# Optimization experiments

Hardware: AMD Instinct MI355X
Metric: run time of the kernel (lower is better)

Reference implementation:

```python
import jax, jax.numpy as jnp
import numpy as np

PAD = 2  # kernel_height // 2 for kernel_height=5


def earth_pad2d(x, ph, pw):
    # circular pad in longitude (last dim), zero pad in latitude (dim 2)
    if pw > 0:
        x = jnp.concatenate([x[..., -pw:], x, x[..., :pw]], axis=-1)
    if ph > 0:
        x = jnp.pad(x, ((0, 0), (0, 0), (ph, ph), (0, 0)))
    return x


def earth_wrap2d(x, w, pad):
    # fold circular overhang of a transposed-conv output back onto width w
    core = x[..., pad:pad + w]
    rw = x.shape[-1] - pad - w  # right overhang (stride-1... here 1)
    core = core.at[..., :rw].add(x[..., pad + w:])
    core = core.at[..., w - pad:].add(x[..., :pad])
    return core


def _conv(x, w, b, stride):
    # torch Conv2d, weight [Cout, Cin, 1, k], VALID padding, stride (1, stride)
    y = jax.lax.conv_general_dilated(x, w, (1, stride), 'VALID',
                                     dimension_numbers=('NCHW', 'OIHW', 'NCHW'))
    return y + b[None, :, None, None]


def _convT(x, w, stride):
    # torch ConvTranspose2d (no bias), weight [Cin, Cout, 1, k], padding 0
    k = w.shape[-1]
    wr = jnp.transpose(jnp.flip(w, axis=(2, 3)), (1, 0, 2, 3))  # -> [Cout, Cin, 1, k]
    return jax.lax.conv_general_dilated(x, wr, (1, 1),
                                        [(0, 0), (k - 1, k - 1)],
                                        lhs_dilation=(1, stride),
                                        dimension_numbers=('NCHW', 'OIHW', 'NCHW'))


def _edge(x, d, p):
    return x[:, :, -p:, :] if d == 1 else x[:, :, :p, :]


def _set_edge(x, d, p, v):
    return x.at[:, :, -p:, :].set(v) if d == 1 else x.at[:, :, :p, :].set(v)


def _forward(strips, wi, wo):
    strips_pad = [earth_pad2d(s, PAD, PAD) for s in strips]
    # center strip inner edges from the adjacent coarser strips (to_inners[0])
    for d in (-1, 1):
        a = _edge(strips[2 + d], -d, PAD)
        a = _convT(a, wi[0], 2)
        a = earth_wrap2d(a, strips[2].shape[3], 2)
        a = earth_pad2d(a, 0, PAD)
        strips_pad[2] = _set_edge(strips_pad[2], d, PAD, a)
    # outer strips: far edge from next coarser (to_inners), near edge from finer (to_outers)
    for mi in (1, 2):
        for d in (-1, 1):
            idx = 2 + d * mi
            sp = strips_pad[idx]
            if mi + 1 <= 2:
                o = _edge(strips[2 + d * (mi + 1)], -d, PAD)
                o = _convT(o, wi[mi], 2)
                o = earth_wrap2d(o, strips[idx].shape[3], 2)
                o = earth_pad2d(o, 0, PAD)
                sp = _set_edge(sp, d, PAD, o)
            en = _edge(strips[2 + d * (mi - 1)], d, PAD)
            en = earth_pad2d(en, 0, 2)
            en = _conv(en, wo[mi - 1][0], wo[mi - 1][1], 2)
            en = earth_pad2d(en, 0, PAD)
            sp = _set_edge(sp, -d, PAD, en)
            strips_pad[idx] = sp
    return tuple(strips_pad)


def setup_inputs():
    key = jax.random.key(0)
    ks = jax.random.split(key, 11)
    B, C, W = 1, 256, 1440
    shapes = [(B, C, 30, W // 4), (B, C, 60, W // 2), (B, C, 180, W),
              (B, C, 60, W // 2), (B, C, 30, W // 4)]
    d = {}
    for i, sh in enumerate(shapes):
        d['s%d' % i] = jax.random.normal(ks[i], sh, dtype=jnp.float32)
    scale = 0.03
    d['wi0'] = jax.random.normal(ks[5], (C, C, 1, 5), dtype=jnp.float32) * scale
    d['wi1'] = jax.random.normal(ks[6], (C, C, 1, 5), dtype=jnp.float32) * scale
    d['wo0'] = jax.random.normal(ks[7], (C, C, 1, 5), dtype=jnp.float32) * scale
    d['bo0'] = jax.random.normal(ks[8], (C,), dtype=jnp.float32) * 0.01
    d['wo1'] = jax.random.normal(ks[9], (C, C, 1, 5), dtype=jnp.float32) * scale
    d['bo1'] = jax.random.normal(ks[10], (C,), dtype=jnp.float32) * 0.01
    return d


def reference(s0, s1, s2, s3, s4, wi0, wi1, wo0, bo0, wo1, bo1):
    return _forward([s0, s1, s2, s3, s4], [wi0, wi1], [(wo0, bo0), (wo1, bo1)])
```

## Files before the change

### kernel.cpp

```cpp
#include <hip/hip_runtime.h>


struct ConvJob {
  const float* x; const float* wt; const float* bias; float* out;
  int Hin, Win, r0, Hout, Wcore, h0, blk_start;
};
struct ConvParams { ConvJob j[8]; };

struct CopyParams {
  const float* in0; const float* in1; const float* in2; const float* in3; const float* in4;
  float* o0; float* o1; float* o2; float* o3; float* o4;
};

struct WTParams { const float* src[4]; float* dst[4]; };

__global__ __launch_bounds__(256) void transpose_all_kernel(WTParams p) {
  int b = blockIdx.x;
  int which = b / 1280;
  int idx = (b - which * 1280) * 256 + threadIdx.x;
  int hi = idx >> 10;
  int icq = hi / 5;
  int k = hi - icq * 5;
  int lo = idx & 1023;
  int oc = lo >> 2;
  int icr = lo & 3;
  int ic = icq * 4 + icr;
  const float* s = p.src[which];
  float v = (which < 2) ? s[(ic * 256 + oc) * 5 + k] : s[(oc * 256 + ic) * 5 + k];
  p.dst[which][idx] = v;
}


template <int NOUT, int NCC>
__device__ __forceinline__ void conv_unit(const ConvJob jb, int local, int t, float* xs,
                                          float bv) {
  int tile = local >> 1;
  int r = local & 1;
  const int Win = jb.Win;
  const int Hout = jb.Hout;
  const float* xrow = jb.x + ((size_t)(t * jb.Hin + jb.r0 + r)) * Win;
  const float* wq = jb.wt + t * 4;
  const int Wop = jb.Wcore + 4;
  float* orow = jb.out + ((size_t)(t * Hout + jb.h0 + r)) * Wop;

  int base0;
  if (NOUT == 8) base0 = 2 * (tile * 8) - 2;
  else           base0 = tile * 8 - 1;
#pragma unroll
  for (int cc = 0; cc < NCC; ++cc) {
    int col = base0 + cc;
    col += (col < 0) ? Win : 0;
    col -= (col >= Win) ? Win : 0;
    xs[cc * 256 + t] = xrow[col];
  }
  __syncthreads();

  float acc[NOUT];
#pragma unroll
  for (int i = 0; i < NOUT; ++i) acc[i] = bv;

#pragma unroll 1
  for (int icq = 0; icq < 64; ++icq) {
    float4 wv[5];
#pragma unroll
    for (int k = 0; k < 5; ++k)
      wv[k] = *(const float4*)(wq + (size_t)(icq * 5 + k) * 1024);
    int ic0 = icq * 4;
#pragma unroll
    for (int cc = 0; cc < NCC; ++cc) {
      float4 xq = *(const float4*)&xs[cc * 256 + ic0];
#pragma unroll
      for (int i = 0; i < NOUT; ++i) {
        int k = (NOUT == 8) ? (cc - 2 * i) : (i + 4 - 2 * cc);
        if (k >= 0 && k < 5) {
          float4 w = wv[k];
          acc[i] += w.x * xq.x + w.y * xq.y + w.z * xq.z + w.w * xq.w;
        }
      }
    }
  }

  __syncthreads();
#pragma unroll
  for (int i = 0; i < NOUT; ++i) xs[i * 257 + t] = acc[i];
  __syncthreads();
  constexpr int SL = NOUT / 2;
  constexpr int OCR = 256 / SL;
  constexpr int RND = 256 / OCR;
  int g0 = (NOUT == 8) ? tile * 8 : tile * 16;
#pragma unroll
  for (int q = 0; q < RND; ++q) {
    int oc = (t / SL) + q * OCR;
    int s = t & (SL - 1);
    float2 v = make_float2(xs[(2 * s) * 257 + oc], xs[(2 * s + 1) * 257 + oc]);
    *(float2*)(jb.out + ((size_t)(oc * Hout + jb.h0 + r)) * Wop + 2 + g0 + 2 * s) = v;
  }
  if (tile == 0) {
    orow[jb.Wcore + 2] = xs[0 * 257 + t];
    orow[jb.Wcore + 3] = xs[1 * 257 + t];
  }
  if (g0 + NOUT == jb.Wcore) {
    orow[0] = xs[(NOUT - 2) * 257 + t];
    orow[1] = xs[(NOUT - 1) * 257 + t];
  }
}

__global__ __launch_bounds__(256, 4) void conv_kernel(ConvParams p) {
  __shared__ float xs[19 * 256];
  int bx = blockIdx.x;
  int t = threadIdx.x;
  if (bx < 540) {
    int ji = (bx >= 450) ? 3 : (bx >= 360) ? 2 : (bx >= 180) ? 1 : 0;
    conv_unit<16, 10>(p.j[ji], bx - p.j[ji].blk_start, t, xs, 0.f);
  } else {
    int j2 = (bx >= 990) ? 7 : (bx >= 900) ? 6 : (bx >= 720) ? 5 : 4;
    conv_unit<8, 19>(p.j[j2], bx - p.j[j2].blk_start, t, xs, p.j[j2].bias[t]);
  }
}


__device__ __forceinline__ float4 pack4(float2 a, float2 b) {
  return make_float4(a.x, a.y, b.x, b.y);
}

template <int H, int W>
__device__ __forceinline__ void copy_row(const float* __restrict__ in,
                                         float* __restrict__ out, int rl, int lane) {
  constexpr int CORE = W / 4;
  int c = rl / H;
  const float* src = in + (size_t)rl * W;
  float* dst = out + (size_t)(rl + c * 4 + 2) * (W + 4);
  int w4 = 1 + lane;
  while (w4 < CORE) {
    int w4b = w4 + 64;
    float2 a0 = *(const float2*)(src + w4 * 4 - 2);
    float2 b0 = *(const float2*)(src + w4 * 4);
    if (w4b < CORE) {
      float2 a1 = *(const float2*)(src + w4b * 4 - 2);
      float2 b1 = *(const float2*)(src + w4b * 4);
      *(float4*)(dst + w4 * 4) = pack4(a0, b0);
      *(float4*)(dst + w4b * 4) = pack4(a1, b1);
    } else {
      *(float4*)(dst + w4 * 4) = pack4(a0, b0);
    }
    w4 += 128;
  }
  if (lane == 0) {
    float2 E = *(const float2*)(src + W - 2);
    float2 F = *(const float2*)(src);
    float4 v = pack4(E, F);
    *(float4*)(dst) = v;
    *(float4*)(dst + W) = v;
  }
}

__device__ __forceinline__ void zero_row(const CopyParams& p, int z, int lane) {
  int strip = z >> 9, cr = z & 511, c = cr >> 1, r = cr & 1;
  float* dst = strip ? p.o4 + (size_t)(c * 34 + 32 + r) * 364
                     : p.o0 + (size_t)(c * 34 + r) * 364;
  for (int w4 = lane; w4 < 91; w4 += 64)
    *(float4*)(dst + w4 * 4) = make_float4(0.f, 0.f, 0.f, 0.f);
}

__device__ __forceinline__ void do_row(const CopyParams& p, int gid, int lane) {
  if (gid < 46080)      copy_row<180, 1440>(p.in2, p.o2, gid, lane);
  else if (gid < 61440) copy_row<60, 720>(p.in1, p.o1, gid - 46080, lane);
  else if (gid < 76800) copy_row<60, 720>(p.in3, p.o3, gid - 61440, lane);
  else if (gid < 84480) copy_row<30, 360>(p.in0, p.o0, gid - 76800, lane);
  else if (gid < 92160) copy_row<30, 360>(p.in4, p.o4, gid - 84480, lane);
  else                  zero_row(p, gid - 92160, lane);
}

__global__ __launch_bounds__(256, 8) void copy_kernel(CopyParams p) {
  int wid = blockIdx.x * 4 + (threadIdx.x >> 6);
  int lane = threadIdx.x & 63;
  for (int gid = wid; gid < 93184; gid += 8192) do_row(p, gid, lane);
}

extern "C" void kernel_launch(void* const* d_in, const int* in_sizes, int n_in,
                              void* d_out, int out_size, void* d_ws, size_t ws_size,
                              hipStream_t stream) {
  const float* s0 = (const float*)d_in[0];
  const float* s1 = (const float*)d_in[1];
  const float* s2 = (const float*)d_in[2];
  const float* s3 = (const float*)d_in[3];
  const float* s4 = (const float*)d_in[4];
  const float* wi0 = (const float*)d_in[5];
  const float* wi1 = (const float*)d_in[6];
  const float* wo0 = (const float*)d_in[7];
  const float* bo0 = (const float*)d_in[8];
  const float* wo1 = (const float*)d_in[9];
  const float* bo1 = (const float*)d_in[10];

  float* out = (float*)d_out;
  float* out0 = out;
  float* out1 = out + 3168256;
  float* out2 = out + 15030272;
  float* out3 = out + 83048448;
  float* out4 = out + 94910464;

  float* wt0 = (float*)d_ws;
  float* wt1 = wt0 + 327680;
  float* wt2 = wt1 + 327680;
  float* wt3 = wt2 + 327680;

  WTParams wp;
  wp.src[0] = wi0; wp.src[1] = wi1; wp.src[2] = wo0; wp.src[3] = wo1;
  wp.dst[0] = wt0; wp.dst[1] = wt1; wp.dst[2] = wt2; wp.dst[3] = wt3;
  transpose_all_kernel<<<5120, 256, 0, stream>>>(wp);

  ConvParams cp;
  cp.j[0] = {s1, wt0, nullptr, out2,  60,  720,  58, 184, 1440,   0,   0};
  cp.j[1] = {s3, wt0, nullptr, out2,  60,  720,   0, 184, 1440, 182, 180};
  cp.j[2] = {s0, wt1, nullptr, out1,  30,  360,  28,  64,  720,   0, 360};
  cp.j[3] = {s4, wt1, nullptr, out3,  30,  360,   0,  64,  720,  62, 450};
  cp.j[4] = {s2, wt2, bo0,     out1, 180, 1440,   0,  64,  720,  62, 540};
  cp.j[5] = {s2, wt2, bo0,     out3, 180, 1440, 178,  64,  720,   0, 720};
  cp.j[6] = {s1, wt3, bo1,     out0,  60,  720,   0,  34,  360,  32, 900};
  cp.j[7] = {s3, wt3, bo1,     out4,  60,  720,  58,  34,  360,   0, 990};
  conv_kernel<<<1080, 256, 0, stream>>>(cp);

  CopyParams kp;
  kp.in0 = s0; kp.in1 = s1; kp.in2 = s2; kp.in3 = s3; kp.in4 = s4;
  kp.o0 = out0; kp.o1 = out1; kp.o2 = out2; kp.o3 = out3; kp.o4 = out4;
  copy_kernel<<<2048, 256, 0, stream>>>(kp);
}
```

Before: 322.6 us.

## Process both edge rows per block, interleave jobs, and prefetch weights

Each conv block now computes both output rows of an edge strip, so every weight float4 loaded is reused for two rows instead of one. Blocks are interleaved across the eight jobs, and tile widths are chosen per job so all jobs use the same number of tiles (720 blocks instead of 1080). The next channel-quad's weights are register-prefetched while the current quad is computed. This doubles the accumulators and the shared-memory footprint, and launch bounds drop occupancy to 2 blocks per SM.

```diff
diff --git a/kernel.cpp b/kernel.cpp
--- a/kernel.cpp
+++ b/kernel.cpp
@@ -3,7 +3,7 @@
 
 struct ConvJob {
   const float* x; const float* wt; const float* bias; float* out;
-  int Hin, Win, r0, Hout, Wcore, h0, blk_start;
+  int Hin, Win, r0, Hout, Wcore, h0;
 };
 struct ConvParams { ConvJob j[8]; };
 
@@ -31,71 +31,26 @@
 }
 
 
-template <int NOUT, int NCC>
-__device__ __forceinline__ void conv_unit(const ConvJob jb, int local, int t, float* xs,
-                                          float bv) {
-  int tile = local >> 1;
-  int r = local & 1;
-  const int Win = jb.Win;
-  const int Hout = jb.Hout;
-  const float* xrow = jb.x + ((size_t)(t * jb.Hin + jb.r0 + r)) * Win;
-  const float* wq = jb.wt + t * 4;
-  const int Wop = jb.Wcore + 4;
-  float* orow = jb.out + ((size_t)(t * Hout + jb.h0 + r)) * Wop;
-
-  int base0;
-  if (NOUT == 8) base0 = 2 * (tile * 8) - 2;
-  else           base0 = tile * 8 - 1;
-#pragma unroll
-  for (int cc = 0; cc < NCC; ++cc) {
-    int col = base0 + cc;
-    col += (col < 0) ? Win : 0;
-    col -= (col >= Win) ? Win : 0;
-    xs[cc * 256 + t] = xrow[col];
-  }
-  __syncthreads();
-
-  float acc[NOUT];
-#pragma unroll
-  for (int i = 0; i < NOUT; ++i) acc[i] = bv;
-
-#pragma unroll 1
-  for (int icq = 0; icq < 64; ++icq) {
-    float4 wv[5];
-#pragma unroll
-    for (int k = 0; k < 5; ++k)
-      wv[k] = *(const float4*)(wq + (size_t)(icq * 5 + k) * 1024);
-    int ic0 = icq * 4;
-#pragma unroll
-    for (int cc = 0; cc < NCC; ++cc) {
-      float4 xq = *(const float4*)&xs[cc * 256 + ic0];
-#pragma unroll
-      for (int i = 0; i < NOUT; ++i) {
-        int k = (NOUT == 8) ? (cc - 2 * i) : (i + 4 - 2 * cc);
-        if (k >= 0 && k < 5) {
-          float4 w = wv[k];
-          acc[i] += w.x * xq.x + w.y * xq.y + w.z * xq.z + w.w * xq.w;
-        }
-      }
-    }
-  }
-
+template <int NOUT>
+__device__ __forceinline__ void epilogue_row(const ConvJob& jb, int g0, int t, int r,
+                                             const float* acc, float* xs) {
   __syncthreads();
 #pragma unroll
   for (int i = 0; i < NOUT; ++i) xs[i * 257 + t] = acc[i];
   __syncthreads();
   constexpr int SL = NOUT / 2;
   constexpr int OCR = 256 / SL;
-  constexpr int RND = 256 / OCR;
-  int g0 = (NOUT == 8) ? tile * 8 : tile * 16;
-#pragma unroll
-  for (int q = 0; q < RND; ++q) {
+  const int Hout = jb.Hout;
+  const int Wop = jb.Wcore + 4;
+#pragma unroll
+  for (int q = 0; q < SL; ++q) {
     int oc = (t / SL) + q * OCR;
     int s = t & (SL - 1);
     float2 v = make_float2(xs[(2 * s) * 257 + oc], xs[(2 * s + 1) * 257 + oc]);
     *(float2*)(jb.out + ((size_t)(oc * Hout + jb.h0 + r)) * Wop + 2 + g0 + 2 * s) = v;
   }
-  if (tile == 0) {
+  float* orow = jb.out + ((size_t)(t * Hout + jb.h0 + r)) * Wop;
+  if (g0 == 0) {
     orow[jb.Wcore + 2] = xs[0 * 257 + t];
     orow[jb.Wcore + 3] = xs[1 * 257 + t];
   }
@@ -105,16 +60,80 @@
   }
 }
 
-__global__ __launch_bounds__(256, 4) void conv_kernel(ConvParams p) {
-  __shared__ float xs[19 * 256];
+template <int NOUT, int NCC, bool TR>
+__device__ __forceinline__ void conv2(const ConvJob jb, int tile, int t, float* xs,
+                                      float bv) {
+  const int Win = jb.Win;
+  int g0 = tile * NOUT;
+  int base0 = TR ? (g0 >> 1) - 1 : 2 * g0 - 2;
+
+#pragma unroll
+  for (int r = 0; r < 2; ++r) {
+    const float* xrow = jb.x + ((size_t)(t * jb.Hin + jb.r0 + r)) * Win;
+#pragma unroll
+    for (int cc = 0; cc < NCC; ++cc) {
+      int col = base0 + cc;
+      col += (col < 0) ? Win : 0;
+      col -= (col >= Win) ? Win : 0;
+      xs[(r * NCC + cc) * 256 + t] = xrow[col];
+    }
+  }
+  __syncthreads();
+
+  float a0[NOUT], a1[NOUT];
+#pragma unroll
+  for (int i = 0; i < NOUT; ++i) { a0[i] = bv; a1[i] = bv; }
+
+  const float* wq = jb.wt + t * 4;
+  float4 wv[5], wn[5];
+#pragma unroll
+  for (int k = 0; k < 5; ++k) wv[k] = *(const float4*)(wq + (size_t)k * 1024);
+
+#pragma unroll 1
+  for (int icq = 0; icq < 64; ++icq) {
+    if (icq < 63) {
+#pragma unroll
+      for (int k = 0; k < 5; ++k)
+        wn[k] = *(const float4*)(wq + (size_t)((icq + 1) * 5 + k) * 1024);
+    }
+    int ic0 = icq * 4;
+#pragma unroll
+    for (int cc = 0; cc < NCC; ++cc) {
+      float4 x0 = *(const float4*)&xs[cc * 256 + ic0];
+      float4 x1 = *(const float4*)&xs[(NCC + cc) * 256 + ic0];
+#pragma unroll
+      for (int i = 0; i < NOUT; ++i) {
+        int k = TR ? (i + 4 - 2 * cc) : (cc - 2 * i);
+        if (k >= 0 && k < 5) {
+          float4 w = wv[k];
+          a0[i] += w.x * x0.x + w.y * x0.y + w.z * x0.z + w.w * x0.w;
+          a1[i] += w.x * x1.x + w.y * x1.y + w.z * x1.z + w.w * x1.w;
+        }
+      }
+    }
+    if (icq < 63) {
+#pragma unroll
+      for (int k = 0; k < 5; ++k) wv[k] = wn[k];
+    }
+  }
+
+  epilogue_row<NOUT>(jb, g0, t, 0, a0, xs);
+  __syncthreads();
+  epilogue_row<NOUT>(jb, g0, t, 1, a1, xs);
+}
+
+__global__ __launch_bounds__(256, 2) void conv_kernel(ConvParams p) {
+  __shared__ float xs[2 * 19 * 256];
   int bx = blockIdx.x;
   int t = threadIdx.x;
-  if (bx < 540) {
-    int ji = (bx >= 450) ? 3 : (bx >= 360) ? 2 : (bx >= 180) ? 1 : 0;
-    conv_unit<16, 10>(p.j[ji], bx - p.j[ji].blk_start, t, xs, 0.f);
-  } else {
-    int j2 = (bx >= 990) ? 7 : (bx >= 900) ? 6 : (bx >= 720) ? 5 : 4;
-    conv_unit<8, 19>(p.j[j2], bx - p.j[j2].blk_start, t, xs, p.j[j2].bias[t]);
+  int job = bx & 7;
+  int tile = bx >> 3;
+  const ConvJob jb = p.j[job];
+  switch (job >> 1) {
+    case 0: conv2<16, 10, true>(jb, tile, t, xs, 0.f); break;
+    case 1: conv2<8, 6, true>(jb, tile, t, xs, 0.f); break;
+    case 2: conv2<8, 19, false>(jb, tile, t, xs, jb.bias[t]); break;
+    default: conv2<4, 11, false>(jb, tile, t, xs, jb.bias[t]); break;
   }
 }
 
@@ -210,15 +229,15 @@
   transpose_all_kernel<<<5120, 256, 0, stream>>>(wp);
 
   ConvParams cp;
-  cp.j[0] = {s1, wt0, nullptr, out2,  60,  720,  58, 184, 1440,   0,   0};
-  cp.j[1] = {s3, wt0, nullptr, out2,  60,  720,   0, 184, 1440, 182, 180};
-  cp.j[2] = {s0, wt1, nullptr, out1,  30,  360,  28,  64,  720,   0, 360};
-  cp.j[3] = {s4, wt1, nullptr, out3,  30,  360,   0,  64,  720,  62, 450};
-  cp.j[4] = {s2, wt2, bo0,     out1, 180, 1440,   0,  64,  720,  62, 540};
-  cp.j[5] = {s2, wt2, bo0,     out3, 180, 1440, 178,  64,  720,   0, 720};
-  cp.j[6] = {s1, wt3, bo1,     out0,  60,  720,   0,  34,  360,  32, 900};
-  cp.j[7] = {s3, wt3, bo1,     out4,  60,  720,  58,  34,  360,   0, 990};
-  conv_kernel<<<1080, 256, 0, stream>>>(cp);
+  cp.j[0] = {s1, wt0, nullptr, out2,  60,  720,  58, 184, 1440,   0};
+  cp.j[1] = {s3, wt0, nullptr, out2,  60,  720,   0, 184, 1440, 182};
+  cp.j[2] = {s0, wt1, nullptr, out1,  30,  360,  28,  64,  720,   0};
+  cp.j[3] = {s4, wt1, nullptr, out3,  30,  360,   0,  64,  720,  62};
+  cp.j[4] = {s2, wt2, bo0,     out1, 180, 1440,   0,  64,  720,  62};
+  cp.j[5] = {s2, wt2, bo0,     out3, 180, 1440, 178,  64,  720,   0};
+  cp.j[6] = {s1, wt3, bo1,     out0,  60,  720,   0,  34,  360,  32};
+  cp.j[7] = {s3, wt3, bo1,     out4,  60,  720,  58,  34,  360,   0};
+  conv_kernel<<<720, 256, 0, stream>>>(cp);
 
   CopyParams kp;
   kp.in0 = s0; kp.in1 = s1; kp.in2 = s2; kp.in3 = s3; kp.in4 = s4;
```

Measured after the change: 370.0 us. 1.15x slower.
